# Performance work log

Measured on AMD Instinct MI355X. Metric: run time of the kernel, lower is better.

The kernel has to match this reference:

```python
import jax, jax.numpy as jnp
import numpy as np

D, H, L, B = 32, 1024, 2, 4096


def _masks(d, h):
    # Sequential (natural) ordering degrees, as in MADE.create_masks
    d_in = jnp.arange(d)                      # input degrees
    d_hid = jnp.arange(h) % (d - 1)           # hidden degrees
    d_out = jnp.arange(d) % d - 1             # output degrees (= arange(d)-1)
    m0 = (d_hid[:, None] >= d_in[None, :]).astype(jnp.float32)   # [H, D]
    mh = (d_hid[:, None] >= d_hid[None, :]).astype(jnp.float32)  # [H, H]
    mo = (d_out[:, None] >= d_hid[None, :]).astype(jnp.float32)  # [D, H]
    mo = jnp.concatenate([mo, mo], axis=0)                       # [2D, H] (mask.repeat(2,1))
    return m0, mh, mo


def setup_inputs() -> dict:
    key = jax.random.key(0)
    ks = jax.random.split(key, 7)
    u = lambda k, shape, fan_in: jax.random.uniform(
        k, shape, minval=-1.0 / np.sqrt(fan_in), maxval=1.0 / np.sqrt(fan_in), dtype=jnp.float32)
    return {
        "z": jax.random.normal(ks[0], (B, D), dtype=jnp.float32),
        "W0": u(ks[1], (H, D), D),
        "b0": u(ks[2], (H,), D),
        "Wh": u(ks[3], (L, H, H), H),
        "bh": u(ks[4], (L, H), H),
        "Wout": u(ks[5], (2 * D, H), H),
        "bout": u(ks[6], (2 * D,), H),
    }


def reference(z, W0, b0, Wh, bh, Wout, bout):
    d = z.shape[1]
    h = W0.shape[0]
    m0, mh, mo = _masks(d, h)
    MW0 = m0 * W0                 # [H, D]
    MWh = mh[None, :, :] * Wh     # [L, H, H]
    MWo = mo * Wout               # [2D, H]

    def net(x):  # masked MLP: [B, D] -> [B, 2D]
        a = jax.nn.relu(x @ MW0.T + b0)
        for i in range(MWh.shape[0]):  # small fixed layer count
            a = jax.nn.relu(a @ MWh[i].T + bh[i])
        return a @ MWo.T + bout

    def step(x, idx):
        theta = net(x)  # [B, 2D]
        mu = jax.lax.dynamic_slice_in_dim(theta, idx, 1, axis=1)[:, 0]
        log_std = jax.lax.dynamic_slice_in_dim(theta, idx + d, 1, axis=1)[:, 0]
        zi = jax.lax.dynamic_slice_in_dim(z, idx, 1, axis=1)[:, 0]
        xi = zi * jnp.exp(log_std) + mu
        x = jax.lax.dynamic_update_slice(x, xi[:, None], (0, idx))
        return x, None

    x0 = jnp.zeros_like(z)
    x, _ = jax.lax.scan(step, x0, jnp.arange(d, dtype=jnp.int32))
    return x
```

## Files before the change

kernel.cpp:

```cpp
#include <hip/hip_runtime.h>
#include <hip/hip_bf16.h>

#define B_ 4096
#define D_ 32
#define H_ 1024
#define CS 512
#define WPK_L 1079296

typedef __attribute__((ext_vector_type(8))) short short8;
typedef __attribute__((ext_vector_type(4))) float floatx4;

#define BAR() __asm__ __volatile__("s_waitcnt lgkmcnt(0)\n\ts_barrier" ::: "memory")

__device__ inline unsigned short f2bf(float f) {
    unsigned u = __float_as_uint(f);
    unsigned r = (u + 0x7FFF + ((u >> 16) & 1)) >> 16;
    return (unsigned short)r;
}

__device__ inline int degs(int hp) { return (hp < 34) ? 0 : (hp - 1) / 33; }
__device__ inline int permf(int hp) {
    int d = degs(hp);
    int r = d ? (hp - 33 * d - 1) : hp;
    return d + 31 * r;
}
__device__ inline int band0i(int idx) {
    int nb0 = (idx == 1) ? 0 : 33 * idx - 32;
    return (nb0 > H_ - 64) ? H_ - 64 : nb0;
}

__global__ __launch_bounds__(256) void prep_all(
        const float* __restrict__ Wh, const float* __restrict__ W0,
        const float* __restrict__ Wout, const float* __restrict__ b0,
        const float* __restrict__ bh,
        unsigned short* __restrict__ Wpk, unsigned short* __restrict__ W0pk,
        unsigned short* __restrict__ Wopk, float* __restrict__ b0p,
        float* __restrict__ bhp) {
    __shared__ float row[H_];
    __shared__ unsigned short rb[H_];
    int b = blockIdx.x, t = threadIdx.x;
    if (b < 2048) {
        int l = b >> 10, np = b & 1023;
        const float* src = Wh + ((size_t)l << 20) + ((size_t)permf(np) << 10);
        ((float4*)row)[t] = ((const float4*)src)[t];
        __syncthreads();
        int dn = degs(np);
        unsigned short o[4];
        #pragma unroll
        for (int j = 0; j < 4; j++) {
            int kp = t * 4 + j;
            o[j] = (dn >= degs(kp)) ? f2bf(row[permf(kp)]) : (unsigned short)0;
        }
        ((ushort4*)rb)[t] = ushort4{o[0], o[1], o[2], o[3]};
        __syncthreads();
        for (int idx = 1; idx < 32; idx++) {
            int nb0 = band0i(idx);
            int j = np - nb0;
            if (j < 0 || j >= 64) continue;
            int nq = (idx + 1) * 4;
            if (t < nq) {
                int c = t >> 2, qd = t & 3;
                size_t base = (size_t)l * WPK_L + (size_t)1024 * (idx - 1) * (idx + 2);
                *(uint4*)(Wpk + base + c * 2048 + j * 32 + qd * 8) =
                    *(const uint4*)(rb + c * 32 + qd * 8);
            }
        }
    } else if (b < 2079) {
        int idx = b - 2047;
        int nb0 = band0i(idx);
        int j = t >> 2, ko = (t & 3) * 8;
        int n = nb0 + j;
        int dn = degs(n);
        const float* srow = W0 + (size_t)permf(n) * 32;
        union { unsigned short o[8]; uint4 v; } u;
        #pragma unroll
        for (int e = 0; e < 8; e++)
            u.o[e] = (dn >= ko + e) ? f2bf(srow[ko + e]) : (unsigned short)0;
        *(uint4*)(W0pk + (idx - 1) * 2048 + j * 32 + ko) = u.v;
    } else if (b < 3103) {
        int bb = b - 2079;
        int idx = bb >> 5, c = bb & 31;
        int ns = idx ? 33 * idx + 1 : 0;
        #pragma unroll
        for (int uu = 0; uu < 2; uu++) {
            int e = t + uu * 256;
            int col = e >> 5, k = e & 31;
            int h = c * 32 + k;
            unsigned short v = 0;
            if (col < 2 && h < ns)
                v = f2bf(Wout[(size_t)(idx + col * 32) * H_ + permf(h)]);
            Wopk[(size_t)bb * 512 + e] = v;
        }
    } else {
        int tt = (b - 3103) * 256 + t;
        int hp = tt & 1023;
        int p = permf(hp);
        if (tt < 1024) b0p[hp] = b0[p];
        else if (tt < 2048) bhp[hp] = bh[p];
        else bhp[1024 + hp] = bh[1024 + p];
    }
}

__device__ inline floatx4 mfma16(short8 a, short8 b, floatx4 c) {
    return __builtin_amdgcn_mfma_f32_16x16x32_bf16(a, b, c, 0, 0, 0);
}

#define BAND_PARTIAL(act, outv) do {                                          \
    const unsigned short* ap_ = (act) + arow;                                 \
    floatx4 x_ = {0.f, 0.f, 0.f, 0.f}, y_ = {0.f, 0.f, 0.f, 0.f};             \
    _Pragma("unroll")                                                         \
    for (int j_ = 0; j_ < 8; j_++) {                                          \
        if (j_ < nch) {                                                       \
            short8 a_ = *(const short8*)(ap_ + (size_t)(c0 + j_) * CS);       \
            if (j_ & 1) y_ = mfma16(a_, rb[j_], y_);                          \
            else        x_ = mfma16(a_, rb[j_], x_);                          \
        }                                                                     \
    }                                                                         \
    outv = x_ + y_;                                                           \
} while (0)

__global__ __launch_bounds__(1024) void mega_kernel(
        const float* __restrict__ z,
        const unsigned short* __restrict__ W0pk,
        const float* __restrict__ b0p,
        const unsigned short* __restrict__ Wpk,
        const float* __restrict__ bhp,
        const unsigned short* __restrict__ Wopk,
        const float* __restrict__ bout,
        float* __restrict__ xout) {
    __shared__ unsigned short aS[3 * 32 * CS];
    __shared__ float xsS[512];
    __shared__ float zsT[512];
    __shared__ floatx4 redS[12 * 64];
    __shared__ float redO[16 * 32];

    const int tid = threadIdx.x;
    const int wave = tid >> 6, lane = tid & 63;
    const int frow = lane & 15, fk = lane >> 4;
    const int arow = frow * 32 + fk * 8;
    const int s = wave & 3, q = wave >> 2;
    const int m0 = blockIdx.x * 16;

    {
        uint4 zz = {0u, 0u, 0u, 0u};
        for (int i = tid; i < 3 * 32 * CS / 8; i += 1024) ((uint4*)aS)[i] = zz;
        if (tid < 128) ((uint4*)xsS)[tid] = zz;
        if (tid < 128) ((uint4*)redO)[tid] = zz;
        if (tid < 128) {
            float4 v = ((const float4*)(z + (size_t)m0 * 32))[tid];
            int row = tid >> 3, c4 = (tid & 7) * 4;
            zsT[(c4 + 0) * 16 + row] = v.x;
            zsT[(c4 + 1) * 16 + row] = v.y;
            zsT[(c4 + 2) * 16 + row] = v.z;
            zsT[(c4 + 3) * 16 + row] = v.w;
        }
    }
    __syncthreads();

    unsigned short* a1 = aS;
    unsigned short* a2 = aS + 32 * CS;
    unsigned short* a3 = aS + 64 * CS;

    short8 rb[8];
    short8 rbf;
    short8 rwo0, rwo1;
    float pb0 = 0.f, pb2 = 0.f, pb3 = 0.f;
    float pbo_m, pbo_s;
    unsigned xaw[4] = {0u, 0u, 0u, 0u};

    rwo0 = *(const short8*)(Wopk + (size_t)((wave * 2) * 16 + frow) * 32 + fk * 8);
    rwo1 = *(const short8*)(Wopk + (size_t)((wave * 2 + 1) * 16 + frow) * 32 + fk * 8);
    pbo_m = bout[0]; pbo_s = bout[D_];

    auto pfL2 = [&](int nidx) {
        const int nkn = nidx + 1;
        const int nk4n = (nkn + 3) >> 2;
        const int c0n = q * nk4n;
        const int c1n = (c0n + nk4n < nkn) ? c0n + nk4n : nkn;
        const int nchn = c1n - c0n;
        const unsigned short* w2 = Wpk + (size_t)1024 * (nidx - 1) * (nidx + 2)
                                 + s * 512 + frow * 32 + fk * 8;
        #pragma unroll
        for (int j = 0; j < 8; j++)
            if (j < nchn) rb[j] = *(const short8*)(w2 + (size_t)(c0n + j) * 2048);
        if (q == 0) {
            const int nb0n = band0i(nidx);
            const int slotn = nb0n + s * 16 + frow;
            rbf = *(const short8*)(W0pk + (nidx - 1) * 2048 + (s * 16 + frow) * 32 + fk * 8);
            pb0 = b0p[slotn];
            pb2 = bhp[slotn];
            pb3 = bhp[H_ + slotn];
        }
    };
    auto pfL3 = [&](int cidx) {
        const int nkn = cidx + 1;
        const int nk4n = (nkn + 3) >> 2;
        const int c0n = q * nk4n;
        const int c1n = (c0n + nk4n < nkn) ? c0n + nk4n : nkn;
        const int nchn = c1n - c0n;
        const unsigned short* w3 = Wpk + WPK_L + (size_t)1024 * (cidx - 1) * (cidx + 2)
                                 + s * 512 + frow * 32 + fk * 8;
        #pragma unroll
        for (int j = 0; j < 8; j++)
            if (j < nchn) rb[j] = *(const short8*)(w3 + (size_t)(c0n + j) * 2048);
    };

    for (int idx = 0; idx < 32; idx++) {
        if (idx > 0) {
            const int nb0 = band0i(idx);
            const int slot = nb0 + s * 16 + frow;
            const int nk = idx + 1;
            const int nk4 = (nk + 3) >> 2;
            const int c0 = q * nk4;
            const int c1m = (c0 + nk4 < nk) ? c0 + nk4 : nk;
            const int nch = c1m - c0;
            const int wsl = (slot >> 5) * CS + (slot & 31);
            const float pb3c = pb3;

            if (q == 0) {
                union { unsigned u[4]; short8 s8; } xc;
                #pragma unroll
                for (int w2 = 0; w2 < 4; ++w2) xc.u[w2] = xaw[w2];
                short8 a = xc.s8;
                floatx4 acc = {0.f, 0.f, 0.f, 0.f};
                acc = mfma16(a, rbf, acc);
                #pragma unroll
                for (int r = 0; r < 4; r++)
                    a1[wsl + (fk * 4 + r) * 32] = f2bf(fmaxf(acc[r] + pb0, 0.f));
            }
            BAR();

            {
                floatx4 p;
                BAND_PARTIAL(a1, p);
                pfL3(idx);
                if (q) redS[((q - 1) * 4 + s) * 64 + lane] = p;
                BAR();
                if (q == 0) {
                    p = p + redS[s * 64 + lane] + redS[(4 + s) * 64 + lane]
                          + redS[(8 + s) * 64 + lane];
                    #pragma unroll
                    for (int r = 0; r < 4; r++)
                        a2[wsl + (fk * 4 + r) * 32] = f2bf(fmaxf(p[r] + pb2, 0.f));
                }
                BAR();
            }

            {
                floatx4 g;
                BAND_PARTIAL(a2, g);
                if (idx < 31) pfL2(idx + 1);
                if (q) redS[((q - 1) * 4 + s) * 64 + lane] = g;
                BAR();
                if (q == 0) {
                    g = g + redS[s * 64 + lane] + redS[(4 + s) * 64 + lane]
                          + redS[(8 + s) * 64 + lane];
                    #pragma unroll
                    for (int r = 0; r < 4; r++)
                        a3[wsl + (fk * 4 + r) * 32] = f2bf(fmaxf(g[r] + pb3c, 0.f));
                }
                BAR();
            }
        } else {
            pfL2(1);
        }

        const float bm = pbo_m, bs = pbo_s;

        {
            floatx4 oacc = {0.f, 0.f, 0.f, 0.f};
            short8 av0 = *(const short8*)(a3 + (wave * 2) * CS + arow);
            short8 av1 = *(const short8*)(a3 + (wave * 2 + 1) * CS + arow);
            oacc = mfma16(av0, rwo0, oacc);
            oacc = mfma16(av1, rwo1, oacc);
            if (idx < 31) {
                rwo0 = *(const short8*)(Wopk + (size_t)(((idx + 1) * 32 + wave * 2) * 16 + frow) * 32 + fk * 8);
                rwo1 = *(const short8*)(Wopk + (size_t)(((idx + 1) * 32 + wave * 2 + 1) * 16 + frow) * 32 + fk * 8);
                pbo_m = bout[idx + 1]; pbo_s = bout[idx + 1 + D_];
            }
            if (frow < 2) {
                #pragma unroll
                for (int r = 0; r < 4; r++)
                    redO[wave * 32 + frow * 16 + fk * 4 + r] = oacc[r];
            }
        }
        BAR();

        {
            const int col = lane & 31;
            const int wbase = (lane >> 5) * 8;
            float v = 0.f;
            #pragma unroll
            for (int w = 0; w < 8; w++) v += redO[(wbase + w) * 32 + col];
            v += __shfl_xor(v, 32);
            float vs = __shfl(v, (lane & 15) + 16);
            float xi = fmaf(zsT[idx * 16 + (lane & 15)], expf(bs + vs), bm + v);
            float xib = __shfl(xi, frow);
            unsigned short xb = f2bf(xib);
            if ((idx >> 3) == fk) {
                const int sh = (idx & 1) * 16;
                const unsigned hb = (unsigned)xb << sh;
                const unsigned msk = ~(0xFFFFu << sh);
                const int wi = (idx >> 1) & 3;
                #pragma unroll
                for (int w2 = 0; w2 < 4; ++w2)
                    if (w2 == wi) xaw[w2] = (xaw[w2] & msk) | hb;
            }
            if (wave == 0 && lane < 16) xsS[lane * 32 + idx] = xi;
        }
    }

    __syncthreads();
    if (tid < 128)
        ((float4*)(xout + (size_t)m0 * 32))[tid] = ((const float4*)xsS)[tid];
}

extern "C" void kernel_launch(void* const* d_in, const int* in_sizes, int n_in,
                              void* d_out, int out_size, void* d_ws, size_t ws_size,
                              hipStream_t stream) {
    const float* z    = (const float*)d_in[0];
    const float* W0   = (const float*)d_in[1];
    const float* b0   = (const float*)d_in[2];
    const float* Wh   = (const float*)d_in[3];
    const float* bh   = (const float*)d_in[4];
    const float* Wout = (const float*)d_in[5];
    const float* bout = (const float*)d_in[6];

    float* x = (float*)d_out;
    unsigned short* Wpk  = (unsigned short*)d_ws;
    unsigned short* W0pk = Wpk + 2 * WPK_L;
    unsigned short* Wopk = W0pk + 31 * 2048;
    float* b0p = (float*)(Wopk + 32 * 32 * 512);
    float* bhp = b0p + H_;

    prep_all<<<3115, 256, 0, stream>>>(Wh, W0, Wout, b0, bh, Wpk, W0pk, Wopk, b0p, bhp);

    mega_kernel<<<B_ / 16, 1024, 0, stream>>>(z, W0pk, b0p, Wpk, bhp, Wopk, bout, x);
}
```

Measured before the change: 197.9 us.

## Split output-layer reduction: idle waves precompute partial sums, q0 waves finish tail

```diff
diff --git a/kernel.cpp b/kernel.cpp
--- a/kernel.cpp
+++ b/kernel.cpp
@@ -132,7 +132,8 @@
     __shared__ float xsS[512];
     __shared__ float zsT[512];
     __shared__ floatx4 redS[12 * 64];
-    __shared__ float redO[16 * 32];
+    __shared__ floatx4 redOv[8 * 64];
+    __shared__ float xL[4 * 16];
 
     const int tid = threadIdx.x;
     const int wave = tid >> 6, lane = tid & 63;
@@ -145,7 +146,7 @@
         uint4 zz = {0u, 0u, 0u, 0u};
         for (int i = tid; i < 3 * 32 * CS / 8; i += 1024) ((uint4*)aS)[i] = zz;
         if (tid < 128) ((uint4*)xsS)[tid] = zz;
-        if (tid < 128) ((uint4*)redO)[tid] = zz;
+        if (tid < 512) ((uint4*)redOv)[tid] = zz;
         if (tid < 128) {
             float4 v = ((const float4*)(z + (size_t)m0 * 32))[tid];
             int row = tid >> 3, c4 = (tid & 7) * 4;
@@ -163,14 +164,13 @@
 
     short8 rb[8];
     short8 rbf;
-    short8 rwo0, rwo1;
+    short8 wof0, wof1;
+    short8 rwo[4];
     float pb0 = 0.f, pb2 = 0.f, pb3 = 0.f;
-    float pbo_m, pbo_s;
+    float pbo_m = 0.f, pbo_s = 0.f;
     unsigned xaw[4] = {0u, 0u, 0u, 0u};
 
-    rwo0 = *(const short8*)(Wopk + (size_t)((wave * 2) * 16 + frow) * 32 + fk * 8);
-    rwo1 = *(const short8*)(Wopk + (size_t)((wave * 2 + 1) * 16 + frow) * 32 + fk * 8);
-    pbo_m = bout[0]; pbo_s = bout[D_];
+    if (q == 0) { pbo_m = bout[0]; pbo_s = bout[D_]; }
 
     auto pfL2 = [&](int nidx) {
         const int nkn = nidx + 1;
@@ -206,6 +206,7 @@
     };
 
     for (int idx = 0; idx < 32; idx++) {
+        const int cb0 = idx - 1;
         if (idx > 0) {
             const int nb0 = band0i(idx);
             const int slot = nb0 + s * 16 + frow;
@@ -221,12 +222,19 @@
                 union { unsigned u[4]; short8 s8; } xc;
                 #pragma unroll
                 for (int w2 = 0; w2 < 4; ++w2) xc.u[w2] = xaw[w2];
-                short8 a = xc.s8;
                 floatx4 acc = {0.f, 0.f, 0.f, 0.f};
-                acc = mfma16(a, rbf, acc);
+                acc = mfma16(xc.s8, rbf, acc);
                 #pragma unroll
                 for (int r = 0; r < 4; r++)
                     a1[wsl + (fk * 4 + r) * 32] = f2bf(fmaxf(acc[r] + pb0, 0.f));
+                wof0 = *(const short8*)(Wopk + (size_t)((idx * 32 + cb0) * 16 + frow) * 32 + fk * 8);
+                wof1 = *(const short8*)(Wopk + (size_t)((idx * 32 + cb0 + 1) * 16 + frow) * 32 + fk * 8);
+            }
+            if (wave >= 8) {
+                const int k4 = (wave - 8) * 4;
+                #pragma unroll
+                for (int j = 0; j < 4; ++j)
+                    rwo[j] = *(const short8*)(Wopk + (size_t)((idx * 32 + k4 + j) * 16 + frow) * 32 + fk * 8);
             }
             BAR();
 
@@ -259,44 +267,52 @@
                     for (int r = 0; r < 4; r++)
                         a3[wsl + (fk * 4 + r) * 32] = f2bf(fmaxf(g[r] + pb3c, 0.f));
                 }
+                if (wave >= 8) {
+                    const int k4 = (wave - 8) * 4;
+                    floatx4 oa = {0.f, 0.f, 0.f, 0.f}, ob = {0.f, 0.f, 0.f, 0.f};
+                    #pragma unroll
+                    for (int j = 0; j < 4; ++j) {
+                        if (k4 + j < cb0) {
+                            short8 a = *(const short8*)(a3 + (size_t)(k4 + j) * CS + arow);
+                            if (j & 1) ob = mfma16(a, rwo[j], ob);
+                            else       oa = mfma16(a, rwo[j], oa);
+                        }
+                    }
+                    redOv[(wave - 8) * 64 + lane] = oa + ob;
+                }
                 BAR();
             }
         } else {
             pfL2(1);
         }
 
-        const float bm = pbo_m, bs = pbo_s;
-
-        {
-            floatx4 oacc = {0.f, 0.f, 0.f, 0.f};
-            short8 av0 = *(const short8*)(a3 + (wave * 2) * CS + arow);
-            short8 av1 = *(const short8*)(a3 + (wave * 2 + 1) * CS + arow);
-            oacc = mfma16(av0, rwo0, oacc);
-            oacc = mfma16(av1, rwo1, oacc);
-            if (idx < 31) {
-                rwo0 = *(const short8*)(Wopk + (size_t)(((idx + 1) * 32 + wave * 2) * 16 + frow) * 32 + fk * 8);
-                rwo1 = *(const short8*)(Wopk + (size_t)(((idx + 1) * 32 + wave * 2 + 1) * 16 + frow) * 32 + fk * 8);
-                pbo_m = bout[idx + 1]; pbo_s = bout[idx + 1 + D_];
-            }
-            if (frow < 2) {
-                #pragma unroll
-                for (int r = 0; r < 4; r++)
-                    redO[wave * 32 + frow * 16 + fk * 4 + r] = oacc[r];
-            }
-        }
-        BAR();
-
-        {
-            const int col = lane & 31;
-            const int wbase = (lane >> 5) * 8;
-            float v = 0.f;
-            #pragma unroll
-            for (int w = 0; w < 8; w++) v += redO[(wbase + w) * 32 + col];
-            v += __shfl_xor(v, 32);
-            float vs = __shfl(v, (lane & 15) + 16);
-            float xi = fmaf(zsT[idx * 16 + (lane & 15)], expf(bs + vs), bm + v);
-            float xib = __shfl(xi, frow);
-            unsigned short xb = f2bf(xib);
+        if (q == 0) {
+            floatx4 od = redOv[lane] + redOv[64 + lane] + redOv[128 + lane]
+                       + redOv[192 + lane] + redOv[256 + lane] + redOv[320 + lane]
+                       + redOv[384 + lane] + redOv[448 + lane];
+            if (idx > 0) {
+                short8 af0 = *(const short8*)(a3 + (size_t)cb0 * CS + arow);
+                short8 af1 = *(const short8*)(a3 + (size_t)(cb0 + 1) * CS + arow);
+                od = mfma16(af0, wof0, od);
+                od = mfma16(af1, wof1, od);
+            }
+            const int base = lane & 48;
+            float ls0 = __shfl(od[0], base + 1);
+            float ls1 = __shfl(od[1], base + 1);
+            float ls2 = __shfl(od[2], base + 1);
+            float ls3 = __shfl(od[3], base + 1);
+            if (frow == 0) {
+                float4 zv = *(const float4*)(zsT + idx * 16 + fk * 4);
+                float4 xi4;
+                xi4.x = fmaf(zv.x, __expf(pbo_s + ls0), pbo_m + od[0]);
+                xi4.y = fmaf(zv.y, __expf(pbo_s + ls1), pbo_m + od[1]);
+                xi4.z = fmaf(zv.z, __expf(pbo_s + ls2), pbo_m + od[2]);
+                xi4.w = fmaf(zv.w, __expf(pbo_s + ls3), pbo_m + od[3]);
+                *(float4*)(xL + wave * 16 + fk * 4) = xi4;
+            }
+            __asm__ __volatile__("s_waitcnt lgkmcnt(0)" ::: "memory");
+            float xiv = xL[wave * 16 + frow];
+            unsigned short xb = f2bf(xiv);
             if ((idx >> 3) == fk) {
                 const int sh = (idx & 1) * 16;
                 const unsigned hb = (unsigned)xb << sh;
@@ -306,7 +322,8 @@
                 for (int w2 = 0; w2 < 4; ++w2)
                     if (w2 == wi) xaw[w2] = (xaw[w2] & msk) | hb;
             }
-            if (wave == 0 && lane < 16) xsS[lane * 32 + idx] = xi;
+            if (wave == 0 && lane < 16) xsS[lane * 32 + idx] = xiv;
+            if (idx < 31) { pbo_m = bout[idx + 1]; pbo_s = bout[idx + 1 + D_]; }
         }
     }
 
```

New measurement: 226.8 us. +14.6%, slower.
